# Kernel tuning notes

Hardware: AMD Instinct MI355X
Metric: run time of the kernel (lower is better)

## Reference

```python
import jax, jax.numpy as jnp
import numpy as np

V = 10000   # vocab_size
H = 512     # hidden_dim
D = 16      # max huffman path depth (pad length)
B = 8192    # batch


def setup_inputs() -> dict:
    key = jax.random.key(0)
    k1, k2, k3, k4, k5 = jax.random.split(key, 5)
    hidden = jax.random.normal(k1, (B, H), dtype=jnp.float32)
    target_words = jax.random.randint(k2, (B,), 0, V)
    # Batched per-word Linear(hidden_dim, path_len, bias=False) weights, padded to D rows.
    weights = jax.random.normal(k3, (V, D, H), dtype=jnp.float32) * 0.02
    # Binary huffman codes (BCE targets), padded to D; lengths are true path lengths.
    codes = jax.random.randint(k4, (V, D), 0, 2).astype(jnp.float32)
    lengths = jax.random.randint(k5, (V,), 8, D + 1)
    return {"hidden": hidden, "target_words": target_words,
            "weights": weights, "codes": codes, "lengths": lengths}


def reference(hidden, target_words, weights, codes, lengths):
    # Gather each sample's word-specific output layer, code, and path length.
    W = weights[target_words]          # [B, D, H]
    t = codes[target_words]            # [B, D]
    L = lengths[target_words]          # [B]
    # Per-sample tiny linear: logits over the huffman path nodes.
    logits = jnp.einsum('bdh,bh->bd', W, hidden)  # [B, D]
    # Stable BCE-with-logits: max(x,0) - x*t + log1p(exp(-|x|))
    bce = jnp.maximum(logits, 0.0) - logits * t + jnp.log1p(jnp.exp(-jnp.abs(logits)))
    mask = (jnp.arange(D)[None, :] < L[:, None]).astype(logits.dtype)  # [B, D]
    # F.binary_cross_entropy_with_logits default reduction='mean' over the path.
    per_word = jnp.sum(bce * mask, axis=1) / L.astype(logits.dtype)    # [B]
    # sum over batch / batch size
    return jnp.mean(per_word)
```

## Files before the change

### kernel.cpp

```cpp
#include <hip/hip_runtime.h>
#include <hip/hip_bf16.h>

#define BATCH 8192
#define HID   512
#define DEPTH 16

__global__ __launch_bounds__(256) void hsm_main_kernel(
    const float* __restrict__ hidden,
    const int*   __restrict__ target,
    const float* __restrict__ weights,
    const float* __restrict__ codes,
    const int*   __restrict__ lengths,
    float*       __restrict__ partial)
{
    const int tid  = threadIdx.x;
    const int wave = tid >> 6;
    const int lane = tid & 63;
    const int b    = blockIdx.x * 4 + wave;
    const int w    = target[b];

    const float4* hrow = (const float4*)(hidden + (size_t)b * HID);
    const float4 h0 = hrow[lane];
    const float4 h1 = hrow[lane + 64];

    const float4* wbase = (const float4*)(weights + (size_t)w * (DEPTH * HID));

    float xmine = 0.0f;
#pragma unroll 4
    for (int d = 0; d < DEPTH; ++d) {
        const float4* wrow = wbase + d * (HID / 4);
        const float4 w0 = wrow[lane];
        const float4 w1 = wrow[lane + 64];
        float acc;
        acc = w0.x * h0.x;
        acc = fmaf(w0.y, h0.y, acc);
        acc = fmaf(w0.z, h0.z, acc);
        acc = fmaf(w0.w, h0.w, acc);
        acc = fmaf(w1.x, h1.x, acc);
        acc = fmaf(w1.y, h1.y, acc);
        acc = fmaf(w1.z, h1.z, acc);
        acc = fmaf(w1.w, h1.w, acc);
#pragma unroll
        for (int m = 32; m >= 1; m >>= 1)
            acc += __shfl_xor(acc, m, 64);
        xmine = (lane == d) ? acc : xmine;
    }

    const int L = lengths[w];
    float v = 0.0f;
    if (lane < DEPTH && lane < L) {
        const float t = codes[(size_t)w * DEPTH + lane];
        const float x = xmine;
        v = fmaxf(x, 0.0f) - x * t + log1pf(__expf(-fabsf(x)));
    }
#pragma unroll
    for (int m = 8; m >= 1; m >>= 1)
        v += __shfl_xor(v, m, 64);

    if (lane == 0)
        partial[b] = v / ((float)L * (float)BATCH);
}

__global__ __launch_bounds__(256) void hsm_reduce_kernel(
    const float* __restrict__ partial, float* __restrict__ out)
{
    __shared__ float sdata[256];
    float s = 0.0f;
    for (int i = threadIdx.x; i < BATCH; i += 256) s += partial[i];
    sdata[threadIdx.x] = s;
    __syncthreads();
#pragma unroll
    for (int stride = 128; stride > 0; stride >>= 1) {
        if (threadIdx.x < stride)
            sdata[threadIdx.x] += sdata[threadIdx.x + stride];
        __syncthreads();
    }
    if (threadIdx.x == 0) out[0] = sdata[0];
}

extern "C" void kernel_launch(void* const* d_in, const int* in_sizes, int n_in,
                              void* d_out, int out_size, void* d_ws, size_t ws_size,
                              hipStream_t stream)
{
    const float* hidden  = (const float*)d_in[0];
    const int*   target  = (const int*)  d_in[1];
    const float* weights = (const float*)d_in[2];
    const float* codes   = (const float*)d_in[3];
    const int*   lengths = (const int*)  d_in[4];
    float* out = (float*)d_out;
    float* partial = (float*)d_ws;

    hsm_main_kernel<<<BATCH / 4, 256, 0, stream>>>(
        hidden, target, weights, codes, lengths, partial);
    hsm_reduce_kernel<<<1, 256, 0, stream>>>(partial, out);
}
```

Baseline: 425.6 us.

## Prefetch weight rows in a 4-deep ring and split warp reductions

Weight rows are now loaded through a 4-slot register ring, so loads for row d+4 are in flight while row d is being reduced. The full 6-step cross-lane reduction per row becomes 2 shuffles per row plus 4 batched 4-step reductions done once at the end. The word index and length are made wave-uniform with readfirstlane, and the four per-wave partials are summed in shared memory so the reduce kernel reads BATCH/4 values. The cost is higher register pressure from the ring and the y array, plus one block-wide barrier.

```diff
diff --git a/kernel.cpp b/kernel.cpp
--- a/kernel.cpp
+++ b/kernel.cpp
@@ -13,11 +13,18 @@
     const int*   __restrict__ lengths,
     float*       __restrict__ partial)
 {
+    __shared__ float sblk[4];
+
     const int tid  = threadIdx.x;
     const int wave = tid >> 6;
     const int lane = tid & 63;
+    const int q    = lane >> 4;
     const int b    = blockIdx.x * 4 + wave;
-    const int w    = target[b];
+
+    int w = target[b];
+    w = __builtin_amdgcn_readfirstlane(w);
+    int L = lengths[w];
+    L = __builtin_amdgcn_readfirstlane(L);
 
     const float4* hrow = (const float4*)(hidden + (size_t)b * HID);
     const float4 h0 = hrow[lane];
@@ -25,12 +32,25 @@
 
     const float4* wbase = (const float4*)(weights + (size_t)w * (DEPTH * HID));
 
-    float xmine = 0.0f;
-#pragma unroll 4
+    float4 wa[4], wb[4];
+#pragma unroll
+    for (int i = 0; i < 4; ++i) {
+        const float4* wr = wbase + i * (HID / 4);
+        wa[i] = wr[lane];
+        wb[i] = wr[lane + 64];
+    }
+
+    float y[4];
+#pragma unroll
     for (int d = 0; d < DEPTH; ++d) {
-        const float4* wrow = wbase + d * (HID / 4);
-        const float4 w0 = wrow[lane];
-        const float4 w1 = wrow[lane + 64];
+        const int s = d & 3;
+        const float4 w0 = wa[s];
+        const float4 w1 = wb[s];
+        if (d + 4 < DEPTH) {
+            const float4* wr = wbase + (d + 4) * (HID / 4);
+            wa[s] = wr[lane];
+            wb[s] = wr[lane + 64];
+        }
         float acc;
         acc = w0.x * h0.x;
         acc = fmaf(w0.y, h0.y, acc);
@@ -40,25 +60,38 @@
         acc = fmaf(w1.y, h1.y, acc);
         acc = fmaf(w1.z, h1.z, acc);
         acc = fmaf(w1.w, h1.w, acc);
-#pragma unroll
-        for (int m = 32; m >= 1; m >>= 1)
-            acc += __shfl_xor(acc, m, 64);
-        xmine = (lane == d) ? acc : xmine;
+        acc += __shfl_xor(acc, 32, 64);
+        acc += __shfl_xor(acc, 16, 64);
+        if (q == (d & 3)) y[d >> 2] = acc;
     }
 
-    const int L = lengths[w];
-    float v = 0.0f;
-    if (lane < DEPTH && lane < L) {
-        const float t = codes[(size_t)w * DEPTH + lane];
-        const float x = xmine;
-        v = fmaxf(x, 0.0f) - x * t + log1pf(__expf(-fabsf(x)));
+#pragma unroll
+    for (int t = 0; t < 4; ++t) {
+        y[t] += __shfl_xor(y[t], 1, 64);
+        y[t] += __shfl_xor(y[t], 2, 64);
+        y[t] += __shfl_xor(y[t], 4, 64);
+        y[t] += __shfl_xor(y[t], 8, 64);
     }
+
+    const float* crow = codes + (size_t)w * DEPTH;
+    float s = 0.0f;
 #pragma unroll
-    for (int m = 8; m >= 1; m >>= 1)
-        v += __shfl_xor(v, m, 64);
+    for (int t = 0; t < 4; ++t) {
+        const int d = 4 * t + q;
+        if (d < L) {
+            const float x = y[t];
+            const float tt = crow[d];
+            s += fmaxf(x, 0.0f) - x * tt + log1pf(__expf(-fabsf(x)));
+        }
+    }
+    s += __shfl_xor(s, 16, 64);
+    s += __shfl_xor(s, 32, 64);
 
     if (lane == 0)
-        partial[b] = v / ((float)L * (float)BATCH);
+        sblk[wave] = s / ((float)L * (float)BATCH);
+    __syncthreads();
+    if (tid == 0)
+        partial[blockIdx.x] = sblk[0] + sblk[1] + sblk[2] + sblk[3];
 }
 
 __global__ __launch_bounds__(256) void hsm_reduce_kernel(
@@ -66,7 +99,7 @@
 {
     __shared__ float sdata[256];
     float s = 0.0f;
-    for (int i = threadIdx.x; i < BATCH; i += 256) s += partial[i];
+    for (int i = threadIdx.x; i < BATCH / 4; i += 256) s += partial[i];
     sdata[threadIdx.x] = s;
     __syncthreads();
 #pragma unroll
```

New measurement: 419.7 us. Within noise of the previous version (-1.4%).
